# Kernel tuning notes

Measured on AMD Instinct MI355X. Metric: run time of the kernel, lower is better.

Reference implementation:

```python
import jax, jax.numpy as jnp
import numpy as np

N, E, B = 20000, 60000, 512
F_IN, ED, H, C = 7, 3, 4, 256
HC = H * C  # 1024
D_MODEL = 1024
EPS_BN = 1e-5


def setup_inputs() -> dict:
    key = jax.random.key(0)
    ks = jax.random.split(key, 24)
    s = 0.05
    inp = {
        'x': jax.random.normal(ks[0], (N, F_IN), jnp.float32),
        'edge_index': jax.random.randint(ks[1], (2, E), 0, N, jnp.int32),
        'edge_attr': jax.random.normal(ks[2], (E, ED), jnp.float32),
        'batch': jnp.sort(jax.random.randint(ks[3], (N,), 0, B, jnp.int32)),
        'w0': jax.random.normal(ks[4], (F_IN, HC), jnp.float32) * s,
        'w_rest': jax.random.normal(ks[5], (3, HC, HC), jnp.float32) * s,
        'w_edge': jax.random.normal(ks[6], (4, ED, HC), jnp.float32) * s,
        'att_src': jax.random.normal(ks[7], (4, H, C), jnp.float32) * s,
        'att_dst': jax.random.normal(ks[8], (4, H, C), jnp.float32) * s,
        'att_edge': jax.random.normal(ks[9], (4, H, C), jnp.float32) * s,
        'bias012': jax.random.normal(ks[10], (3, HC), jnp.float32) * s,
        'bias3': jax.random.normal(ks[11], (C,), jnp.float32) * s,
        'bn_gamma': jnp.ones((3, HC), jnp.float32),
        'bn_beta': jnp.zeros((3, HC), jnp.float32),
        'bn_mean': jnp.zeros((3, HC), jnp.float32),
        'bn_var': jnp.ones((3, HC), jnp.float32),
        'gate_w': jax.random.normal(ks[12], (C, 1), jnp.float32) * s,
        'gate_b': jnp.zeros((1,), jnp.float32),
        'proj_w': jax.random.normal(ks[13], (C, D_MODEL), jnp.float32) * s,
        'proj_b': jnp.zeros((D_MODEL,), jnp.float32),
    }
    return inp


def _gat_layer(x, ei, ea, W, We, a_s, a_d, a_e, bias, concat):
    # PyG GATConv with edge_dim, add_self_loops=True (fill_value='mean'), eval mode (no dropout)
    n = x.shape[0]
    sl = jnp.arange(n, dtype=ei.dtype)
    ea_mean = ea.mean(axis=0)
    ei = jnp.concatenate([ei, jnp.stack([sl, sl])], axis=1)            # [2, E+N]
    ea = jnp.concatenate([ea, jnp.broadcast_to(ea_mean, (n, ea.shape[1]))], axis=0)
    h = (x @ W).reshape(n, H, C)                                       # [N,H,C]
    alpha_src = jnp.einsum('nhc,hc->nh', h, a_s)
    alpha_dst = jnp.einsum('nhc,hc->nh', h, a_d)
    eh = (ea @ We).reshape(-1, H, C)
    alpha_e = jnp.einsum('ehc,hc->eh', eh, a_e)
    src, dst = ei[0], ei[1]
    alpha = jax.nn.leaky_relu(alpha_src[src] + alpha_dst[dst] + alpha_e, 0.2)  # [E+N,H]
    amax = jax.ops.segment_max(alpha, dst, num_segments=n)
    alpha = jnp.exp(alpha - amax[dst])
    denom = jax.ops.segment_sum(alpha, dst, num_segments=n)
    alpha = alpha / (denom[dst] + 1e-16)
    msg = h[src] * alpha[:, :, None]                                   # [E+N,H,C]
    out = jax.ops.segment_sum(msg, dst, num_segments=n)                # [N,H,C]
    out = out.reshape(n, H * C) if concat else out.mean(axis=1)
    return out + bias


def reference(x, edge_index, edge_attr, batch, w0, w_rest, w_edge, att_src, att_dst,
              att_edge, bias012, bias3, bn_gamma, bn_beta, bn_mean, bn_var,
              gate_w, gate_b, proj_w, proj_b):
    h = x
    for i in range(4):
        W = w0 if i == 0 else w_rest[i - 1]
        concat = i < 3
        b = bias012[i] if concat else bias3
        h = _gat_layer(h, edge_index, edge_attr, W, w_edge[i],
                       att_src[i], att_dst[i], att_edge[i], b, concat)
        if i < 3:
            # BatchNorm1d in eval mode, then ReLU (dropout is identity in eval)
            h = (h - bn_mean[i]) * (bn_gamma[i] / jnp.sqrt(bn_var[i] + EPS_BN)) + bn_beta[i]
            h = jax.nn.relu(h)
    # AttentionalAggregation: segment softmax over gate scores, weighted sum per graph
    gate = h @ gate_w + gate_b                                         # [N,1]
    gmax = jax.ops.segment_max(gate, batch, num_segments=B)
    g = jnp.exp(gate - gmax[batch])
    gsum = jax.ops.segment_sum(g, batch, num_segments=B)
    w = g / (gsum[batch] + 1e-16)
    graph = jax.ops.segment_sum(w * h, batch, num_segments=B)          # [B,256]
    return graph @ proj_w + proj_b                                     # [B,1024]
```

## Files before the change

kernel.cpp:

```cpp
#include <hip/hip_runtime.h>
#include <math.h>

#define NN 20000
#define NP 20480
#define EE 60000
#define BB 512
#define HC 1024
#define HH 4
#define CC 256

typedef _Float16 f16;
typedef f16 half8 __attribute__((ext_vector_type(8)));
typedef f16 f16x4 __attribute__((ext_vector_type(4)));
typedef float floatx4 __attribute__((ext_vector_type(4)));
typedef float floatx16 __attribute__((ext_vector_type(16)));

__device__ __forceinline__ size_t af_off(int n, int c) {
    int mblk = n >> 7, rr = n & 127;
    int iter = c >> 5, kc = c & 31;
    int kh = kc >> 4, kg = (kc >> 3) & 1, e = kc & 7;
    return ((((size_t)(mblk * 32 + iter) * 2 + kh) * 4 + (rr >> 5)) * 64 +
            (kg * 32 + (rr & 31))) * 8 + e;
}

__device__ __forceinline__ int node_remap(int bid) {
    return (bid >> 3) + (bid & 7) * 2500;
}

__device__ __forceinline__ void gload16(const f16* g, f16* l) {
    __builtin_amdgcn_global_load_lds((const __attribute__((address_space(1))) void*)g,
                                     (__attribute__((address_space(3))) void*)l, 16, 0, 0);
}

__global__ void ehist_kernel(const float* __restrict__ ea, const int* __restrict__ ei,
                             float* sums, int* counts, int E_) {
    int e = blockIdx.x * 256 + threadIdx.x;
    float s0 = 0.f, s1 = 0.f, s2 = 0.f;
    if (e < E_) {
        atomicAdd(&counts[ei[E_ + e]], 1);
        s0 = ea[e * 3 + 0];
        s1 = ea[e * 3 + 1];
        s2 = ea[e * 3 + 2];
    }
    for (int o = 32; o; o >>= 1) {
        s0 += __shfl_down(s0, o);
        s1 += __shfl_down(s1, o);
        s2 += __shfl_down(s2, o);
    }
    if ((threadIdx.x & 63) == 0) {
        atomicAdd(&sums[0], s0);
        atomicAdd(&sums[1], s1);
        atomicAdd(&sums[2], s2);
    }
}

__global__ void scan1_kernel(const int* __restrict__ counts, int* __restrict__ partial,
                             int* __restrict__ psums, int n) {
    __shared__ int sdata[256];
    int t = threadIdx.x;
    int i = blockIdx.x * 256 + t;
    int v = (i < n) ? counts[i] : 0;
    sdata[t] = v;
    __syncthreads();
#pragma unroll
    for (int off = 1; off < 256; off <<= 1) {
        int tmp = (t >= off) ? sdata[t - off] : 0;
        __syncthreads();
        sdata[t] += tmp;
        __syncthreads();
    }
    if (i < n) partial[i] = sdata[t];
    if (t == 255) psums[blockIdx.x] = sdata[255];
}

__global__ void scan2_kernel(int* __restrict__ psums, int nb) {
    __shared__ int sdata[128];
    int t = threadIdx.x;
    sdata[t] = (t < nb) ? psums[t] : 0;
    __syncthreads();
#pragma unroll
    for (int off = 1; off < 128; off <<= 1) {
        int tmp = (t >= off) ? sdata[t - off] : 0;
        __syncthreads();
        sdata[t] += tmp;
        __syncthreads();
    }
    if (t < nb) psums[t] = (t == 0) ? 0 : sdata[t - 1];
}

__global__ void scan3_kernel(const int* __restrict__ partial, const int* __restrict__ psums,
                             int* __restrict__ indptr, int n) {
    int i = blockIdx.x * 256 + threadIdx.x;
    if (i == 0) indptr[0] = 0;
    if (i < n) indptr[i + 1] = partial[i] + psums[blockIdx.x];
}

__global__ void scatter_kernel(const int* __restrict__ ei, const int* __restrict__ indptr,
                               int* fill, int* sorted, int* sdst, int E_) {
    int e = blockIdx.x * 256 + threadIdx.x;
    if (e >= E_) return;
    int d = ei[E_ + e];
    int pos = indptr[d] + atomicAdd(&fill[d], 1);
    sorted[pos] = e;
    sdst[pos] = d;
}

__global__ void bptr_kernel(const int* __restrict__ batch, int* bptr, int n, int nb) {
    int i = blockIdx.x * 256 + threadIdx.x;
    if (i >= n) return;
    int b = batch[i];
    if (i == 0) {
        for (int bb = 0; bb <= b; bb++) bptr[bb] = 0;
    } else {
        int pb = batch[i - 1];
        if (pb != b) {
            for (int bb = pb + 1; bb <= b; bb++) bptr[bb] = i;
        }
    }
    if (i == n - 1) {
        for (int bb = b + 1; bb <= nb; bb++) bptr[bb] = n;
    }
}

__global__ void prep0_kernel(const float* __restrict__ w_rest, f16* __restrict__ Bf,
                             const float* __restrict__ att_src,
                             const float* __restrict__ att_dst,
                             const float* __restrict__ w0,
                             const float* __restrict__ bias012, const float* __restrict__ bn_g,
                             const float* __restrict__ bn_b, const float* __restrict__ bn_m,
                             const float* __restrict__ bn_v,
                             const float* __restrict__ w_edge,
                             const float* __restrict__ att_edge,
                             const float* __restrict__ ea_sums,
                             float* __restrict__ wsv, float* __restrict__ wdv,
                             float* __restrict__ w0s, float* __restrict__ w0d,
                             float2* __restrict__ bnss,
                             float* __restrict__ Mmat, float* __restrict__ ae_self,
                             float invE) {
    int bid = blockIdx.x;
    int t = threadIdx.x;
    if (bid < 768) {
        __shared__ float tile[64][65];
        int bx = (bid & 15) * 64;
        int by = ((bid >> 4) & 15) * 64;
        int l = bid >> 8;
        int tr = t >> 6, tc = t & 63;
#pragma unroll
        for (int i = 0; i < 16; i++) {
            int r = by + i * 4 + tr;
            tile[i * 4 + tr][tc] = w_rest[(size_t)l * 1048576 + (size_t)r * 1024 + bx + tc];
        }
        __syncthreads();
        f16* bl = Bf + (size_t)l * 1048576;
#pragma unroll
        for (int ii = 0; ii < 2; ii++) {
            int idx = ii * 256 + t;
            int nl = idx >> 3, kg8 = idx & 7;
            int n = bx + nl, k = by + kg8 * 8;
            half8 v;
#pragma unroll
            for (int e = 0; e < 8; e++) v[e] = (f16)tile[kg8 * 8 + e][nl];
            *(half8*)&bl[af_off(n, k)] = v;
        }
    } else if (bid < 3840) {
        int b = bid - 768;
        int l = b >> 10, k = b & 1023;
        int hp = t >> 6, lane = t & 63;
        int col = hp * 256 + lane * 4;
        const float* wrow = w_rest + (size_t)l * 1048576 + (size_t)k * 1024;
        float4 w4 = *(const float4*)&wrow[col];
        float4 a4 = *(const float4*)&att_src[(l + 1) * HC + col];
        float4 d4 = *(const float4*)&att_dst[(l + 1) * HC + col];
        float sp = w4.x * a4.x + w4.y * a4.y + w4.z * a4.z + w4.w * a4.w;
        float dp = w4.x * d4.x + w4.y * d4.y + w4.z * d4.z + w4.w * d4.w;
        for (int m = 1; m < 64; m <<= 1) {
            sp += __shfl_xor(sp, m);
            dp += __shfl_xor(dp, m);
        }
        if (lane == 0) {
            wsv[((size_t)l * 1024 + k) * 4 + hp] = sp;
            wdv[((size_t)l * 1024 + k) * 4 + hp] = dp;
        }
    } else if (bid < 3847) {
        int f = bid - 3840;
        int hp = t >> 6, lane = t & 63;
        int col = hp * 256 + lane * 4;
        float4 w4 = *(const float4*)&w0[f * HC + col];
        float4 a4 = *(const float4*)&att_src[col];
        float4 d4 = *(const float4*)&att_dst[col];
        float sp = w4.x * a4.x + w4.y * a4.y + w4.z * a4.z + w4.w * a4.w;
        float dp = w4.x * d4.x + w4.y * d4.y + w4.z * d4.z + w4.w * d4.w;
        for (int m = 1; m < 64; m <<= 1) {
            sp += __shfl_xor(sp, m);
            dp += __shfl_xor(dp, m);
        }
        if (lane == 0) {
            w0s[f * 4 + hp] = sp;
            w0d[f * 4 + hp] = dp;
        }
    } else if (bid < 3859) {
        int i = (bid - 3847) * 256 + t;
        if (i < 3 * HC) {
            float s = bn_g[i] * rsqrtf(bn_v[i] + 1e-5f);
            float2 o;
            o.x = s;
            o.y = (bias012[i] - bn_m[i]) * s + bn_b[i];
            bnss[i] = o;
        }
    } else {
        __shared__ float red[256];
        __shared__ float Ms[12];
        int l = bid - 3859;
        for (int dh = 0; dh < 12; dh++) {
            int d = dh >> 2, hh = dh & 3;
            float v = w_edge[l * 3072 + d * HC + hh * CC + t] *
                      att_edge[l * HC + hh * CC + t];
            red[t] = v;
            __syncthreads();
            for (int o = 128; o; o >>= 1) {
                if (t < o) red[t] += red[t + o];
                __syncthreads();
            }
            if (t == 0) {
                Ms[dh] = red[0];
                Mmat[l * 12 + dh] = red[0];
            }
            __syncthreads();
        }
        if (t < 4) {
            float v = 0.f;
            for (int d = 0; d < 3; d++) v += ea_sums[d] * invE * Ms[d * 4 + t];
            ae_self[l * 4 + t] = v;
        }
    }
}

__global__ void prep2_kernel(const int* __restrict__ ei, const int* __restrict__ sorted,
                             const float* __restrict__ ea, const float* __restrict__ Mmat,
                             int* __restrict__ ssrc, float* __restrict__ aeh_pk,
                             const float* __restrict__ x, const float* __restrict__ w0s,
                             const float* __restrict__ w0d, float* __restrict__ asrc,
                             float* __restrict__ adst, float* __restrict__ xpad) {
    int bid = blockIdx.x;
    int t = threadIdx.x;
    if (bid < 235) {
        int idx = bid * 256 + t;
        if (idx >= EE) return;
        int eid = sorted[idx];
        ssrc[idx] = ei[eid];
        float a0 = ea[eid * 3 + 0], a1 = ea[eid * 3 + 1], a2 = ea[eid * 3 + 2];
#pragma unroll
        for (int l = 0; l < 4; l++) {
#pragma unroll
            for (int h = 0; h < 4; h++) {
                aeh_pk[(size_t)idx * 16 + l * 4 + h] =
                    a0 * Mmat[l * 12 + h] + a1 * Mmat[l * 12 + 4 + h] +
                    a2 * Mmat[l * 12 + 8 + h];
            }
        }
    } else {
        int n = (bid - 235) * 256 + t;
        if (n >= NN) return;
        float xr[7];
#pragma unroll
        for (int f = 0; f < 7; f++) xr[f] = x[n * 7 + f];
        float4 p0, p1;
        p0.x = xr[0]; p0.y = xr[1]; p0.z = xr[2]; p0.w = xr[3];
        p1.x = xr[4]; p1.y = xr[5]; p1.z = xr[6]; p1.w = 0.f;
        *(float4*)&xpad[(size_t)n * 8] = p0;
        *(float4*)&xpad[(size_t)n * 8 + 4] = p1;
#pragma unroll
        for (int hp = 0; hp < 4; hp++) {
            float s = 0.f, d = 0.f;
#pragma unroll
            for (int f = 0; f < 7; f++) {
                s += xr[f] * w0s[f * 4 + hp];
                d += xr[f] * w0d[f * 4 + hp];
            }
            asrc[n * 4 + hp] = s;
            adst[n * 4 + hp] = d;
        }
    }
}

__global__ void edgep_kernel(const int* __restrict__ ssrc, const int* __restrict__ sdst,
                             const float* __restrict__ aeh_pk, const float* __restrict__ asrc,
                             const float* __restrict__ adst, float* __restrict__ pe,
                             int layer) {
    int i = blockIdx.x * 256 + threadIdx.x;
    if (i >= EE) return;
    int src = ssrc[i];
    int dst = sdst[i];
    float4 a = *(const float4*)&asrc[(size_t)src * 4];
    float4 d = *(const float4*)&adst[(size_t)dst * 4];
    float4 m = *(const float4*)&aeh_pk[(size_t)i * 16 + layer * 4];
    float r[4] = {a.x + d.x + m.x, a.y + d.y + m.y, a.z + d.z + m.z, a.w + d.w + m.w};
    float4 o;
#pragma unroll
    for (int k = 0; k < 4; k++) {
        float v = (r[k] > 0.f) ? r[k] : 0.2f * r[k];
        (&o.x)[k] = __expf(v);
    }
    *(float4*)&pe[(size_t)i * 4] = o;
}

__global__ void agg0x_kernel(const float* __restrict__ xpad, const float* __restrict__ asrc,
                             const float* __restrict__ adst, const float* __restrict__ ae_self,
                             const int* __restrict__ ssrc, const float* __restrict__ pe,
                             const int* __restrict__ indptr, float* __restrict__ xagg) {
    int n = blockIdx.x * 256 + threadIdx.x;
    if (n >= NN) return;
    float4 as4 = *(const float4*)&asrc[(size_t)n * 4];
    float4 ad4 = *(const float4*)&adst[(size_t)n * 4];
    float adl[4] = {ad4.x, ad4.y, ad4.z, ad4.w};
    float asl[4] = {as4.x, as4.y, as4.z, as4.w};
    float4 x0 = *(const float4*)&xpad[(size_t)n * 8];
    float4 x1 = *(const float4*)&xpad[(size_t)n * 8 + 4];
    float xr[7] = {x0.x, x0.y, x0.z, x0.w, x1.x, x1.y, x1.z};
    float denom[4];
    float xa[4][7];
#pragma unroll
    for (int h = 0; h < 4; h++) {
        float r = asl[h] + adl[h] + ae_self[h];
        r = (r > 0.f) ? r : 0.2f * r;
        float p = __expf(r);
        denom[h] = p;
#pragma unroll
        for (int f = 0; f < 7; f++) xa[h][f] = p * xr[f];
    }
    int s = indptr[n], e = indptr[n + 1];
    for (int idx = s; idx < e; idx++) {
        int src = ssrc[idx];
        float4 pv = *(const float4*)&pe[(size_t)idx * 4];
        float pl[4] = {pv.x, pv.y, pv.z, pv.w};
        float4 s0 = *(const float4*)&xpad[(size_t)src * 8];
        float4 s1 = *(const float4*)&xpad[(size_t)src * 8 + 4];
        float xs[7] = {s0.x, s0.y, s0.z, s0.w, s1.x, s1.y, s1.z};
#pragma unroll
        for (int h = 0; h < 4; h++) {
            denom[h] += pl[h];
#pragma unroll
            for (int f = 0; f < 7; f++) xa[h][f] += pl[h] * xs[f];
        }
    }
#pragma unroll
    for (int h = 0; h < 4; h++) {
        float inv = 1.0f / (denom[h] + 1e-16f);
#pragma unroll
        for (int f = 0; f < 7; f++) xagg[(size_t)n * 28 + h * 7 + f] = xa[h][f] * inv;
    }
}

__global__ void gemm7f_kernel(const float* __restrict__ xagg, const float* __restrict__ w0,
                              const float2* __restrict__ bnss, const float* __restrict__ wsv,
                              const float* __restrict__ wdv, f16* __restrict__ outAf,
                              float* __restrict__ asrc_n, float* __restrict__ adst_n) {
    __shared__ float xs[32][29];
    __shared__ float red[4][32][8];
    int bid = blockIdx.x;
    int t = threadIdx.x;
    int n0 = bid * 32;
    int mblk = bid >> 2, rg = bid & 3;
    for (int i = t; i < 896; i += 256) xs[i / 28][i % 28] = xagg[(size_t)n0 * 28 + i];
    __syncthreads();
    int w = t >> 6, lane = t & 63;
    int lr = lane & 31, kg = lane >> 5;
    float x7[7];
#pragma unroll
    for (int f = 0; f < 7; f++) x7[f] = xs[lr][w * 7 + f];
    float sp[4] = {0.f, 0.f, 0.f, 0.f}, dp[4] = {0.f, 0.f, 0.f, 0.f};
#pragma unroll
    for (int p = 0; p < 16; p++) {
        int iter = w * 8 + (p >> 1);
        int kh = p & 1;
        int c0 = iter * 32 + (kh * 2 + kg) * 8;
        float dot[8];
#pragma unroll
        for (int e = 0; e < 8; e++) dot[e] = 0.f;
#pragma unroll
        for (int f = 0; f < 7; f++) {
            float4 wa = *(const float4*)&w0[f * HC + c0];
            float4 wb = *(const float4*)&w0[f * HC + c0 + 4];
            dot[0] += x7[f] * wa.x; dot[1] += x7[f] * wa.y;
            dot[2] += x7[f] * wa.z; dot[3] += x7[f] * wa.w;
            dot[4] += x7[f] * wb.x; dot[5] += x7[f] * wb.y;
            dot[6] += x7[f] * wb.z; dot[7] += x7[f] * wb.w;
        }
        half8 o;
#pragma unroll
        for (int e = 0; e < 8; e++) {
            int j = c0 + e;
            float2 ss = bnss[j];
            float val = fmaxf(fmaf(dot[e], ss.x, ss.y), 0.f);
            o[e] = (f16)val;
            float4 w4s = *(const float4*)&wsv[(size_t)j * 4];
            float4 w4d = *(const float4*)&wdv[(size_t)j * 4];
            sp[0] += val * w4s.x; sp[1] += val * w4s.y;
            sp[2] += val * w4s.z; sp[3] += val * w4s.w;
            dp[0] += val * w4d.x; dp[1] += val * w4d.y;
            dp[2] += val * w4d.z; dp[3] += val * w4d.w;
        }
        size_t off = ((((size_t)(mblk * 32 + iter) * 2 + kh) * 4 + rg) * 64 + lane) * 8;
        *(half8*)&outAf[off] = o;
    }
#pragma unroll
    for (int q = 0; q < 4; q++) {
        sp[q] += __shfl_xor(sp[q], 32);
        dp[q] += __shfl_xor(dp[q], 32);
    }
    if (kg == 0) {
#pragma unroll
        for (int q = 0; q < 4; q++) {
            red[w][lr][q] = sp[q];
            red[w][lr][4 + q] = dp[q];
        }
    }
    __syncthreads();
    {
        int lr2 = t >> 3, q = t & 7;
        float v = red[0][lr2][q] + red[1][lr2][q] + red[2][lr2][q] + red[3][lr2][q];
        if (q < 4) asrc_n[(size_t)(n0 + lr2) * 4 + q] = v;
        else adst_n[(size_t)(n0 + lr2) * 4 + (q - 4)] = v;
    }
}

#define EPB 235
__global__ __launch_bounds__(256) void gemmep_kernel(
    const f16* __restrict__ Af, const f16* __restrict__ Bf, f16* __restrict__ C16,
    const int* __restrict__ ssrc, const int* __restrict__ sdst,
    const float* __restrict__ aeh_pk, const float* __restrict__ asrc,
    const float* __restrict__ adst, float* __restrict__ pe, int layer) {
    __shared__ __align__(16) f16 lds[16384];
    int t = threadIdx.x;
    int bid = blockIdx.x;
    if (bid < EPB) {
        int i = bid * 256 + t;
        if (i >= EE) return;
        int src = ssrc[i];
        int dst = sdst[i];
        float4 a = *(const float4*)&asrc[(size_t)src * 4];
        float4 d = *(const float4*)&adst[(size_t)dst * 4];
        float4 m = *(const float4*)&aeh_pk[(size_t)i * 16 + layer * 4];
        float r[4] = {a.x + d.x + m.x, a.y + d.y + m.y, a.z + d.z + m.z, a.w + d.w + m.w};
        float4 o;
#pragma unroll
        for (int k = 0; k < 4; k++) {
            float v = (r[k] > 0.f) ? r[k] : 0.2f * r[k];
            (&o.x)[k] = __expf(v);
        }
        *(float4*)&pe[(size_t)i * 4] = o;
        return;
    }
    int gid = bid - EPB;
    int w = t >> 6, lane = t & 63;
    int g = gid >> 6, rblk = gid & 63;
    int nblk = rblk >> 3;
    int mblk = g * 8 + (rblk & 7);
    int rg0 = (w >> 1) * 2;
    int cg0 = (w & 1) * 2;

    floatx16 acc[2][2];
#pragma unroll
    for (int i = 0; i < 2; i++)
#pragma unroll
        for (int j = 0; j < 2; j++) acc[i][j] = (floatx16)(0.f);

    const f16* ga0 = Af + (size_t)mblk * 131072 + w * 1024 + lane * 8;
    const f16* gb0 = Bf + (size_t)nblk * 131072 + w * 1024 + lane * 8;

    auto STAGE = [&](int it, int b) {
        const f16* ga = ga0 + (size_t)it * 4096;
        const f16* gb = gb0 + (size_t)it * 4096;
        f16* la = &lds[b * 8192 + w * 1024 + lane * 8];
        f16* lb = &lds[b * 8192 + 4096 + w * 1024 + lane * 8];
        gload16(ga, la);
        gload16(ga + 512, la + 512);
        gload16(gb, lb);
        gload16(gb + 512, lb + 512);
    };
    auto COMPUTE = [&](int b) {
        half8 afr[2][2], bfr[2][2];
#pragma unroll
        for (int kh = 0; kh < 2; kh++) {
#pragma unroll
            for (int i = 0; i < 2; i++) {
                afr[kh][i] = *(const half8*)&lds[b * 8192 + kh * 2048 + (rg0 + i) * 512 +
                                                 lane * 8];
                bfr[kh][i] = *(const half8*)&lds[b * 8192 + 4096 + kh * 2048 +
                                                 (cg0 + i) * 512 + lane * 8];
            }
        }
#pragma unroll
        for (int kh = 0; kh < 2; kh++)
#pragma unroll
            for (int i = 0; i < 2; i++)
#pragma unroll
                for (int j = 0; j < 2; j++)
                    acc[i][j] = __builtin_amdgcn_mfma_f32_32x32x16_f16(bfr[kh][j], afr[kh][i],
                                                                       acc[i][j], 0, 0, 0);
    };

    STAGE(0, 0);
    __syncthreads();
#pragma unroll 1
    for (int k2 = 0; k2 < 16; k2++) {
        int i0 = k2 * 2;
        STAGE(i0 + 1, 1);
        COMPUTE(0);
        __syncthreads();
        if (i0 + 2 < 32) STAGE(i0 + 2, 0);
        COMPUTE(1);
        __syncthreads();
    }

    int fr32 = lane & 31, kg = lane >> 5;
#pragma unroll
    for (int i = 0; i < 2; i++) {
        int row = mblk * 128 + rg0 * 32 + i * 32 + fr32;
#pragma unroll
        for (int j = 0; j < 2; j++) {
#pragma unroll
            for (int gq = 0; gq < 4; gq++) {
                f16x4 o;
#pragma unroll
                for (int r = 0; r < 4; r++) o[r] = (f16)acc[i][j][gq * 4 + r];
                *(f16x4*)&C16[(size_t)row * HC + nblk * 128 + cg0 * 32 + j * 32 + gq * 8 +
                              kg * 4] = o;
            }
        }
    }
}

__global__ void agg_kernel(const f16* __restrict__ h16, const float* __restrict__ asrc,
                           const float* __restrict__ adst, const float* __restrict__ ae_self,
                           const int* __restrict__ ssrc, const float* __restrict__ pe,
                           const int* __restrict__ indptr, const float2* __restrict__ bnss,
                           const float* __restrict__ wsv, const float* __restrict__ wdv,
                           const float* __restrict__ bias3, const float* __restrict__ gw,
                           const float* __restrict__ gb, f16* __restrict__ out16,
                           float* __restrict__ asrc_n, float* __restrict__ adst_n,
                           float* __restrict__ out3, float* __restrict__ gate,
                           int layer, int concat) {
    __shared__ float buf[1024];
    __shared__ float red[32];
    int n = node_remap(blockIdx.x);
    int t = threadIdx.x;
    int h = t >> 6, lane = t & 63;
    int c4 = t * 4;

    float r = asrc[n * 4 + h] + adst[n * 4 + h] + ae_self[layer * 4 + h];
    r = (r > 0.f) ? r : 0.2f * r;
    float p = __expf(r);
    float denom = p;
    float ax, ay, az, aw;
    {
        f16x4 v = *(const f16x4*)&h16[(size_t)n * HC + c4];
        ax = p * (float)v[0]; ay = p * (float)v[1];
        az = p * (float)v[2]; aw = p * (float)v[3];
    }
    int s = indptr[n], epos = indptr[n + 1];
    for (int base = s; base < epos; base += 4) {
        int rem = epos - base;
        int src[4];
        float pv[4];
#pragma unroll
        for (int j = 0; j < 4; j++) {
            if (j < rem) {
                src[j] = ssrc[base + j];
                pv[j] = pe[(size_t)(base + j) * 4 + h];
            } else {
                src[j] = n;
                pv[j] = 0.f;
            }
        }
        f16x4 u[4];
#pragma unroll
        for (int j = 0; j < 4; j++) u[j] = *(const f16x4*)&h16[(size_t)src[j] * HC + c4];
#pragma unroll
        for (int j = 0; j < 4; j++) {
            denom += pv[j];
            ax += pv[j] * (float)u[j][0];
            ay += pv[j] * (float)u[j][1];
            az += pv[j] * (float)u[j][2];
            aw += pv[j] * (float)u[j][3];
        }
    }
    float inv = 1.0f / (denom + 1e-16f);
    ax *= inv; ay *= inv; az *= inv; aw *= inv;

    if (concat) {
        float vals[4] = {ax, ay, az, aw};
        f16x4 o;
        float sp[4] = {0.f, 0.f, 0.f, 0.f}, dp[4] = {0.f, 0.f, 0.f, 0.f};
#pragma unroll
        for (int k = 0; k < 4; k++) {
            int j = c4 + k;
            float2 ss = bnss[j];
            float val = fmaxf(fmaf(vals[k], ss.x, ss.y), 0.f);
            o[k] = (f16)val;
            float4 w4s = *(const float4*)&wsv[(size_t)j * 4];
            float4 w4d = *(const float4*)&wdv[(size_t)j * 4];
            sp[0] += val * w4s.x; sp[1] += val * w4s.y;
            sp[2] += val * w4s.z; sp[3] += val * w4s.w;
            dp[0] += val * w4d.x; dp[1] += val * w4d.y;
            dp[2] += val * w4d.z; dp[3] += val * w4d.w;
        }
        *(f16x4*)&out16[af_off(n, c4)] = o;
#pragma unroll
        for (int m = 1; m < 64; m <<= 1) {
#pragma unroll
            for (int j = 0; j < 4; j++) {
                sp[j] += __shfl_xor(sp[j], m);
                dp[j] += __shfl_xor(dp[j], m);
            }
        }
        if (lane == 0) {
#pragma unroll
            for (int j = 0; j < 4; j++) {
                red[h * 8 + j] = sp[j];
                red[h * 8 + 4 + j] = dp[j];
            }
        }
        __syncthreads();
        if (t < 8) {
            float v = red[t] + red[8 + t] + red[16 + t] + red[24 + t];
            if (t < 4) asrc_n[n * 4 + t] = v;
            else adst_n[n * 4 + (t - 4)] = v;
        }
    } else {
        buf[c4 + 0] = ax;
        buf[c4 + 1] = ay;
        buf[c4 + 2] = az;
        buf[c4 + 3] = aw;
        __syncthreads();
        if (t < 64) {
            float gpart = 0.f;
#pragma unroll
            for (int k = 0; k < 4; k++) {
                int c = t * 4 + k;
                float v2 = 0.25f * (buf[c] + buf[256 + c] + buf[512 + c] + buf[768 + c]) +
                           bias3[c];
                out3[(size_t)n * CC + c] = v2;
                gpart += v2 * gw[c];
            }
            for (int o = 32; o; o >>= 1) gpart += __shfl_down(gpart, o);
            if (t == 0) gate[n] = gpart + gb[0];
        }
    }
}

__global__ void graphagg_kernel(const float* __restrict__ gate, const float* __restrict__ h3,
                                const int* __restrict__ bptr, float* __restrict__ graph) {
    __shared__ float red[256];
    __shared__ float wn[256];
    int b = blockIdx.x, t = threadIdx.x;
    int s = bptr[b], epos = bptr[b + 1];
    float m = -3.4e38f;
    for (int n = s + t; n < epos; n += 256) m = fmaxf(m, gate[n]);
    red[t] = m;
    __syncthreads();
    for (int o = 128; o; o >>= 1) {
        if (t < o) red[t] = fmaxf(red[t], red[t + o]);
        __syncthreads();
    }
    float mval = red[0];
    __syncthreads();
    float sum = 0.f;
    for (int n = s + t; n < epos; n += 256) sum += __expf(gate[n] - mval);
    red[t] = sum;
    __syncthreads();
    for (int o = 128; o; o >>= 1) {
        if (t < o) red[t] += red[t + o];
        __syncthreads();
    }
    float ssum = red[0];
    __syncthreads();
    float acc = 0.f;
    for (int base = s; base < epos; base += 256) {
        int n = base + t;
        wn[t] = (n < epos) ? __expf(gate[n] - mval) : 0.f;
        __syncthreads();
        int cnt = min(256, epos - base);
        for (int j = 0; j < cnt; j++) acc += wn[j] * h3[(size_t)(base + j) * CC + t];
        __syncthreads();
    }
    graph[b * CC + t] = acc / (ssum + 1e-16f);
}

__global__ void proj_kernel(const float* __restrict__ graph, const float* __restrict__ pw,
                            const float* __restrict__ pb, float* __restrict__ out) {
    __shared__ float g[8][256];
    int b = blockIdx.x, t = threadIdx.x;
#pragma unroll
    for (int r = 0; r < 8; r++) g[r][t] = graph[(size_t)(b * 8 + r) * 256 + t];
    __syncthreads();
    float acc[8][4];
#pragma unroll
    for (int r = 0; r < 8; r++)
#pragma unroll
        for (int q = 0; q < 4; q++) acc[r][q] = pb[t + q * 256];
    for (int c = 0; c < 256; c++) {
        float w[4];
#pragma unroll
        for (int q = 0; q < 4; q++) w[q] = pw[(size_t)c * 1024 + t + q * 256];
#pragma unroll
        for (int r = 0; r < 8; r++) {
            float gv = g[r][c];
#pragma unroll
            for (int q = 0; q < 4; q++) acc[r][q] += gv * w[q];
        }
    }
#pragma unroll
    for (int r = 0; r < 8; r++)
#pragma unroll
        for (int q = 0; q < 4; q++)
            out[(size_t)(b * 8 + r) * 1024 + t + q * 256] = acc[r][q];
}

extern "C" void kernel_launch(void* const* d_in, const int* in_sizes, int n_in,
                              void* d_out, int out_size, void* d_ws, size_t ws_size,
                              hipStream_t stream) {
    const float* x = (const float*)d_in[0];
    const int* ei = (const int*)d_in[1];
    const float* ea = (const float*)d_in[2];
    const int* batch = (const int*)d_in[3];
    const float* w0 = (const float*)d_in[4];
    const float* w_rest = (const float*)d_in[5];
    const float* w_edge = (const float*)d_in[6];
    const float* att_src = (const float*)d_in[7];
    const float* att_dst = (const float*)d_in[8];
    const float* att_edge = (const float*)d_in[9];
    const float* bias012 = (const float*)d_in[10];
    const float* bias3 = (const float*)d_in[11];
    const float* bn_g = (const float*)d_in[12];
    const float* bn_b = (const float*)d_in[13];
    const float* bn_m = (const float*)d_in[14];
    const float* bn_v = (const float*)d_in[15];
    const float* gate_w = (const float*)d_in[16];
    const float* gate_b = (const float*)d_in[17];
    const float* proj_w = (const float*)d_in[18];
    const float* proj_b = (const float*)d_in[19];
    float* out = (float*)d_out;

    float* ws = (float*)d_ws;
    size_t off = 0;
    f16* h_lin = (f16*)(ws + off); off += (size_t)NP * HC / 2;
    f16* h_af = (f16*)(ws + off); off += (size_t)NP * HC / 2;
    float* h3 = ws + off; off += (size_t)NN * CC;
    f16* Bf = (f16*)(ws + off); off += (size_t)3 * HC * HC / 2;
    float* xpad = ws + off; off += (size_t)NN * 8;
    float* asrcA = ws + off; off += (size_t)NN * 4;
    float* adstA = ws + off; off += (size_t)NN * 4;
    float* asrcB = ws + off; off += (size_t)NN * 4;
    float* adstB = ws + off; off += (size_t)NN * 4;
    float* wsv = ws + off; off += (size_t)3 * HC * 4;
    float* wdv = ws + off; off += (size_t)3 * HC * 4;
    float* w0s = ws + off; off += 28;
    float* w0d = ws + off; off += 28;
    float2* bnss = (float2*)(ws + off); off += (size_t)3 * HC * 2;
    float* aeh_pk = ws + off; off += (size_t)EE * 16;
    float* pbuf = ws + off; off += (size_t)EE * 4;
    float* xagg = ws + off; off += (size_t)NN * 28;
    float* gate = ws + off; off += (size_t)NN;
    float* graph = ws + off; off += (size_t)BB * CC;
    float* ea_sums = ws + off; off += 4;
    float* Mmat = ws + off; off += 48;
    float* ae_self = ws + off; off += 16;
    int* counts = (int*)(ws + off); off += NN;
    int* partial = (int*)(ws + off); off += NN;
    int* psums = (int*)(ws + off); off += 128;
    int* indptr = (int*)(ws + off); off += NN + 1;
    int* fill = (int*)(ws + off); off += NN;
    int* sorted = (int*)(ws + off); off += EE;
    int* ssrc = (int*)(ws + off); off += EE;
    int* sdst = (int*)(ws + off); off += EE;
    int* bptr = (int*)(ws + off); off += BB + 1;

    hipMemsetAsync(ea_sums, 0, 4 * sizeof(float), stream);
    hipMemsetAsync(counts, 0, NN * sizeof(int), stream);
    hipMemsetAsync(fill, 0, NN * sizeof(int), stream);

    ehist_kernel<<<(EE + 255) / 256, 256, 0, stream>>>(ea, ei, ea_sums, counts, EE);
    int nblk = (NN + 255) / 256;
    scan1_kernel<<<nblk, 256, 0, stream>>>(counts, partial, psums, NN);
    scan2_kernel<<<1, 128, 0, stream>>>(psums, nblk);
    scan3_kernel<<<nblk, 256, 0, stream>>>(partial, psums, indptr, NN);
    scatter_kernel<<<(EE + 255) / 256, 256, 0, stream>>>(ei, indptr, fill, sorted, sdst, EE);
    bptr_kernel<<<(NN + 255) / 256, 256, 0, stream>>>(batch, bptr, NN, BB);
    prep0_kernel<<<3863, 256, 0, stream>>>(w_rest, Bf, att_src, att_dst, w0, bias012, bn_g,
                                           bn_b, bn_m, bn_v, w_edge, att_edge, ea_sums,
                                           wsv, wdv, w0s, w0d, bnss, Mmat, ae_self,
                                           1.0f / EE);
    prep2_kernel<<<235 + nblk, 256, 0, stream>>>(ei, sorted, ea, Mmat, ssrc, aeh_pk,
                                                 x, w0s, w0d, asrcA, adstA, xpad);

    edgep_kernel<<<(EE + 255) / 256, 256, 0, stream>>>(ssrc, sdst, aeh_pk, asrcA, adstA,
                                                       pbuf, 0);
    agg0x_kernel<<<nblk, 256, 0, stream>>>(xpad, asrcA, adstA, ae_self, ssrc,
                                           pbuf, indptr, xagg);
    gemm7f_kernel<<<NN / 32, 256, 0, stream>>>(xagg, w0, bnss, wsv, wdv, h_af, asrcB,
                                               adstB);

    float* asrc_cur = asrcB;
    float* adst_cur = adstB;
    float* asrc_nxt = asrcA;
    float* adst_nxt = adstA;
    for (int i = 1; i < 4; i++) {
        gemmep_kernel<<<EPB + (NP / 128) * (HC / 128), 256, 0, stream>>>(
            h_af, Bf + (size_t)(i - 1) * HC * HC, h_lin,
            ssrc, sdst, aeh_pk, asrc_cur, adst_cur, pbuf, i);
        agg_kernel<<<NN, 256, 0, stream>>>(
            h_lin, asrc_cur, adst_cur, ae_self, ssrc, pbuf, indptr, bnss + (size_t)i * HC,
            wsv + (size_t)i * HC * 4, wdv + (size_t)i * HC * 4, bias3, gate_w, gate_b,
            h_af, asrc_nxt, adst_nxt, h3, gate, i, (i < 3) ? 1 : 0);
        float* tmp = asrc_cur; asrc_cur = asrc_nxt; asrc_nxt = tmp;
        tmp = adst_cur; adst_cur = adst_nxt; adst_nxt = tmp;
    }

    graphagg_kernel<<<BB, 256, 0, stream>>>(gate, h3, bptr, graph);
    proj_kernel<<<BB / 8, 256, 0, stream>>>(graph, proj_w, proj_b, out);
}
```

Before: 623.7 us.

## Triple-buffer GEMM staging, fuse bptr into ehist, split-K proj, trim agg padding

The fp16 GEMM mainloop moves from double to triple LDS buffering, with one barrier per iteration, a partial vmcnt wait and raised wave priority during compute. This is meant to hide global-to-LDS load latency. Separately, the bptr computation is merged into the ehist launch to save a kernel launch. The projection is split four ways over the input dimension with atomicAdd into a zeroed output, giving more blocks at the cost of an extra memset and atomics. Padded neighbour loads in the aggregation are now skipped with conditionals instead of using dummy entries.

```diff
diff --git a/kernel.cpp b/kernel.cpp
--- a/kernel.cpp
+++ b/kernel.cpp
@@ -33,24 +33,44 @@
 }
 
 __global__ void ehist_kernel(const float* __restrict__ ea, const int* __restrict__ ei,
-                             float* sums, int* counts, int E_) {
-    int e = blockIdx.x * 256 + threadIdx.x;
-    float s0 = 0.f, s1 = 0.f, s2 = 0.f;
-    if (e < E_) {
-        atomicAdd(&counts[ei[E_ + e]], 1);
-        s0 = ea[e * 3 + 0];
-        s1 = ea[e * 3 + 1];
-        s2 = ea[e * 3 + 2];
-    }
-    for (int o = 32; o; o >>= 1) {
-        s0 += __shfl_down(s0, o);
-        s1 += __shfl_down(s1, o);
-        s2 += __shfl_down(s2, o);
-    }
-    if ((threadIdx.x & 63) == 0) {
-        atomicAdd(&sums[0], s0);
-        atomicAdd(&sums[1], s1);
-        atomicAdd(&sums[2], s2);
+                             const int* __restrict__ batch, float* sums, int* counts,
+                             int* bptr, int E_) {
+    int bid = blockIdx.x;
+    int t = threadIdx.x;
+    if (bid < 235) {
+        int e = bid * 256 + t;
+        float s0 = 0.f, s1 = 0.f, s2 = 0.f;
+        if (e < E_) {
+            atomicAdd(&counts[ei[E_ + e]], 1);
+            s0 = ea[e * 3 + 0];
+            s1 = ea[e * 3 + 1];
+            s2 = ea[e * 3 + 2];
+        }
+        for (int o = 32; o; o >>= 1) {
+            s0 += __shfl_down(s0, o);
+            s1 += __shfl_down(s1, o);
+            s2 += __shfl_down(s2, o);
+        }
+        if ((t & 63) == 0) {
+            atomicAdd(&sums[0], s0);
+            atomicAdd(&sums[1], s1);
+            atomicAdd(&sums[2], s2);
+        }
+    } else {
+        int i = (bid - 235) * 256 + t;
+        if (i >= NN) return;
+        int b = batch[i];
+        if (i == 0) {
+            for (int bb = 0; bb <= b; bb++) bptr[bb] = 0;
+        } else {
+            int pb = batch[i - 1];
+            if (pb != b) {
+                for (int bb = pb + 1; bb <= b; bb++) bptr[bb] = i;
+            }
+        }
+        if (i == NN - 1) {
+            for (int bb = b + 1; bb <= BB; bb++) bptr[bb] = NN;
+        }
     }
 }
 
@@ -103,23 +123,6 @@
     int pos = indptr[d] + atomicAdd(&fill[d], 1);
     sorted[pos] = e;
     sdst[pos] = d;
-}
-
-__global__ void bptr_kernel(const int* __restrict__ batch, int* bptr, int n, int nb) {
-    int i = blockIdx.x * 256 + threadIdx.x;
-    if (i >= n) return;
-    int b = batch[i];
-    if (i == 0) {
-        for (int bb = 0; bb <= b; bb++) bptr[bb] = 0;
-    } else {
-        int pb = batch[i - 1];
-        if (pb != b) {
-            for (int bb = pb + 1; bb <= b; bb++) bptr[bb] = i;
-        }
-    }
-    if (i == n - 1) {
-        for (int bb = b + 1; bb <= nb; bb++) bptr[bb] = n;
-    }
 }
 
 __global__ void prep0_kernel(const float* __restrict__ w_rest, f16* __restrict__ Bf,
@@ -430,7 +433,7 @@
     const int* __restrict__ ssrc, const int* __restrict__ sdst,
     const float* __restrict__ aeh_pk, const float* __restrict__ asrc,
     const float* __restrict__ adst, float* __restrict__ pe, int layer) {
-    __shared__ __align__(16) f16 lds[16384];
+    __shared__ __align__(16) f16 lds[24576];
     int t = threadIdx.x;
     int bid = blockIdx.x;
     if (bid < EPB) {
@@ -471,12 +474,11 @@
     auto STAGE = [&](int it, int b) {
         const f16* ga = ga0 + (size_t)it * 4096;
         const f16* gb = gb0 + (size_t)it * 4096;
-        f16* la = &lds[b * 8192 + w * 1024 + lane * 8];
-        f16* lb = &lds[b * 8192 + 4096 + w * 1024 + lane * 8];
-        gload16(ga, la);
-        gload16(ga + 512, la + 512);
-        gload16(gb, lb);
-        gload16(gb + 512, lb + 512);
+        f16* base = &lds[b * 8192 + w * 1024 + lane * 8];
+        gload16(ga, base);
+        gload16(ga + 512, base + 512);
+        gload16(gb, base + 4096);
+        gload16(gb + 512, base + 4608);
     };
     auto COMPUTE = [&](int b) {
         half8 afr[2][2], bfr[2][2];
@@ -501,17 +503,28 @@
     };
 
     STAGE(0, 0);
-    __syncthreads();
+    STAGE(1, 1);
+    int cb = 0, sb = 2;
 #pragma unroll 1
-    for (int k2 = 0; k2 < 16; k2++) {
-        int i0 = k2 * 2;
-        STAGE(i0 + 1, 1);
-        COMPUTE(0);
-        __syncthreads();
-        if (i0 + 2 < 32) STAGE(i0 + 2, 0);
-        COMPUTE(1);
-        __syncthreads();
-    }
+    for (int k = 0; k < 31; k++) {
+        asm volatile("s_waitcnt vmcnt(4)" ::: "memory");
+        __builtin_amdgcn_s_barrier();
+        __builtin_amdgcn_sched_barrier(0);
+        if (k < 30) {
+            STAGE(k + 2, sb);
+            sb = (sb == 2) ? 0 : sb + 1;
+        }
+        __builtin_amdgcn_s_setprio(1);
+        COMPUTE(cb);
+        __builtin_amdgcn_s_setprio(0);
+        cb = (cb == 2) ? 0 : cb + 1;
+    }
+    asm volatile("s_waitcnt vmcnt(0)" ::: "memory");
+    __builtin_amdgcn_s_barrier();
+    __builtin_amdgcn_sched_barrier(0);
+    __builtin_amdgcn_s_setprio(1);
+    COMPUTE(cb);
+    __builtin_amdgcn_s_setprio(0);
 
     int fr32 = lane & 31, kg = lane >> 5;
 #pragma unroll
@@ -568,21 +581,22 @@
             if (j < rem) {
                 src[j] = ssrc[base + j];
                 pv[j] = pe[(size_t)(base + j) * 4 + h];
-            } else {
-                src[j] = n;
-                pv[j] = 0.f;
             }
         }
         f16x4 u[4];
 #pragma unroll
-        for (int j = 0; j < 4; j++) u[j] = *(const f16x4*)&h16[(size_t)src[j] * HC + c4];
-#pragma unroll
         for (int j = 0; j < 4; j++) {
-            denom += pv[j];
-            ax += pv[j] * (float)u[j][0];
-            ay += pv[j] * (float)u[j][1];
-            az += pv[j] * (float)u[j][2];
-            aw += pv[j] * (float)u[j][3];
+            if (j < rem) u[j] = *(const f16x4*)&h16[(size_t)src[j] * HC + c4];
+        }
+#pragma unroll
+        for (int j = 0; j < 4; j++) {
+            if (j < rem) {
+                denom += pv[j];
+                ax += pv[j] * (float)u[j][0];
+                ay += pv[j] * (float)u[j][1];
+                az += pv[j] * (float)u[j][2];
+                aw += pv[j] * (float)u[j][3];
+            }
         }
     }
     float inv = 1.0f / (denom + 1e-16f);
@@ -689,20 +703,33 @@
 
 __global__ void proj_kernel(const float* __restrict__ graph, const float* __restrict__ pw,
                             const float* __restrict__ pb, float* __restrict__ out) {
-    __shared__ float g[8][256];
-    int b = blockIdx.x, t = threadIdx.x;
-#pragma unroll
-    for (int r = 0; r < 8; r++) g[r][t] = graph[(size_t)(b * 8 + r) * 256 + t];
+    __shared__ float g[8][64];
+    int bid = blockIdx.x;
+    int grp = bid >> 2, cch = bid & 3;
+    int t = threadIdx.x;
+    int c0 = cch * 64;
+    for (int i = t; i < 512; i += 256) {
+        int r = i >> 6, c = i & 63;
+        g[r][c] = graph[(size_t)(grp * 8 + r) * 256 + c0 + c];
+    }
     __syncthreads();
     float acc[8][4];
 #pragma unroll
     for (int r = 0; r < 8; r++)
 #pragma unroll
-        for (int q = 0; q < 4; q++) acc[r][q] = pb[t + q * 256];
-    for (int c = 0; c < 256; c++) {
+        for (int q = 0; q < 4; q++) acc[r][q] = 0.f;
+    if (cch == 0) {
+#pragma unroll
+        for (int q = 0; q < 4; q++) {
+            float b = pb[t + q * 256];
+#pragma unroll
+            for (int r = 0; r < 8; r++) acc[r][q] += b;
+        }
+    }
+    for (int c = 0; c < 64; c++) {
         float w[4];
 #pragma unroll
-        for (int q = 0; q < 4; q++) w[q] = pw[(size_t)c * 1024 + t + q * 256];
+        for (int q = 0; q < 4; q++) w[q] = pw[(size_t)(c0 + c) * 1024 + t + q * 256];
 #pragma unroll
         for (int r = 0; r < 8; r++) {
             float gv = g[r][c];
@@ -714,7 +741,7 @@
     for (int r = 0; r < 8; r++)
 #pragma unroll
         for (int q = 0; q < 4; q++)
-            out[(size_t)(b * 8 + r) * 1024 + t + q * 256] = acc[r][q];
+            atomicAdd(&out[(size_t)(grp * 8 + r) * 1024 + t + q * 256], acc[r][q]);
 }
 
 extern "C" void kernel_launch(void* const* d_in, const int* in_sizes, int n_in,
@@ -779,14 +806,14 @@
     hipMemsetAsync(ea_sums, 0, 4 * sizeof(float), stream);
     hipMemsetAsync(counts, 0, NN * sizeof(int), stream);
     hipMemsetAsync(fill, 0, NN * sizeof(int), stream);
-
-    ehist_kernel<<<(EE + 255) / 256, 256, 0, stream>>>(ea, ei, ea_sums, counts, EE);
+    hipMemsetAsync(out, 0, (size_t)BB * 1024 * sizeof(float), stream);
+
     int nblk = (NN + 255) / 256;
+    ehist_kernel<<<235 + nblk, 256, 0, stream>>>(ea, ei, batch, ea_sums, counts, bptr, EE);
     scan1_kernel<<<nblk, 256, 0, stream>>>(counts, partial, psums, NN);
     scan2_kernel<<<1, 128, 0, stream>>>(psums, nblk);
     scan3_kernel<<<nblk, 256, 0, stream>>>(partial, psums, indptr, NN);
     scatter_kernel<<<(EE + 255) / 256, 256, 0, stream>>>(ei, indptr, fill, sorted, sdst, EE);
-    bptr_kernel<<<(NN + 255) / 256, 256, 0, stream>>>(batch, bptr, NN, BB);
     prep0_kernel<<<3863, 256, 0, stream>>>(w_rest, Bf, att_src, att_dst, w0, bias012, bn_g,
                                            bn_b, bn_m, bn_v, w_edge, att_edge, ea_sums,
                                            wsv, wdv, w0s, w0d, bnss, Mmat, ae_self,
@@ -818,5 +845,5 @@
     }
 
     graphagg_kernel<<<BB, 256, 0, stream>>>(gate, h3, bptr, graph);
-    proj_kernel<<<BB / 8, 256, 0, stream>>>(graph, proj_w, proj_b, out);
-}
+    proj_kernel<<<256, 256, 0, stream>>>(graph, proj_w, proj_b, out);
+}
```

After: 594.7 us. 1.05x faster.
